# Kernel tuning notes

Measured on AMD Instinct MI355X. Metric: run time of the kernel, lower is better.

Reference implementation:

```python
import jax, jax.numpy as jnp
import numpy as np

SCALE = 16.0 / 8.0  # alpha / rank


def setup_inputs() -> dict:
    key = jax.random.key(0)
    ks = jax.random.split(key, 5)
    d_in, d_out, rank = 4096, 4096, 8
    x = jax.random.normal(ks[0], (4, 2048, d_in), dtype=jnp.float32)
    base_weight = jax.random.normal(ks[1], (d_out, d_in), dtype=jnp.float32) * 0.02
    lora_A = jax.random.normal(ks[2], (rank, d_in), dtype=jnp.float32) * 0.02
    lora_B = jax.random.normal(ks[3], (d_out, rank), dtype=jnp.float32) * 0.02
    bias = jax.random.normal(ks[4], (d_out,), dtype=jnp.float32) * 0.02
    return {"x": x, "base_weight": base_weight, "lora_A": lora_A,
            "lora_B": lora_B, "bias": bias}


def reference(x, base_weight, lora_A, lora_B, bias):
    # weight = base + scale * (B @ A)   -> [d_out, d_in]
    weight = base_weight + SCALE * (lora_B @ lora_A)
    # F.linear: x @ weight.T + bias
    return jnp.einsum('bsi,oi->bso', x, weight) + bias
```

## Files before the change

### kernel.cpp

```cpp
#include <hip/hip_runtime.h>
#include <hip/hip_bf16.h>
#include <cstdio>


using bf16   = __bf16;
using bf16x8 = __attribute__((ext_vector_type(8))) __bf16;
using f32x4  = __attribute__((ext_vector_type(4))) float;

#define BM 256
#define BN 256
#define BK 64

__global__ __launch_bounds__(256) void prep_x(const float* __restrict__ x,
                                              bf16* __restrict__ Xb, long n8) {
    const long stride = (long)gridDim.x * blockDim.x;
    for (long i = (long)blockIdx.x * blockDim.x + threadIdx.x; i < n8; i += stride) {
        const float4 a = reinterpret_cast<const float4*>(x)[2 * i];
        const float4 b = reinterpret_cast<const float4*>(x)[2 * i + 1];
        bf16x8 o;
        o[0] = (bf16)a.x; o[1] = (bf16)a.y; o[2] = (bf16)a.z; o[3] = (bf16)a.w;
        o[4] = (bf16)b.x; o[5] = (bf16)b.y; o[6] = (bf16)b.z; o[7] = (bf16)b.w;
        reinterpret_cast<bf16x8*>(Xb)[i] = o;
    }
}

__global__ __launch_bounds__(256) void prep_w(const float* __restrict__ base,
                                              const float* __restrict__ A,
                                              const float* __restrict__ Bm,
                                              bf16* __restrict__ Wb,
                                              int K, int rank, float scale) {
    const int o = blockIdx.x;
    float br[8];
    const int rr = rank < 8 ? rank : 8;
    for (int r = 0; r < rr; ++r) br[r] = scale * Bm[(size_t)o * rank + r];

    const float* brow = base + (size_t)o * K;
    bf16*        wrow = Wb + (size_t)o * K;

    for (int c = threadIdx.x * 8; c < K; c += 256 * 8) {
        float4 s0 = *reinterpret_cast<const float4*>(brow + c);
        float4 s1 = *reinterpret_cast<const float4*>(brow + c + 4);
        if (rank == 8) {
#pragma unroll
            for (int r = 0; r < 8; ++r) {
                const float4 a0 = *reinterpret_cast<const float4*>(A + (size_t)r * K + c);
                const float4 a1 = *reinterpret_cast<const float4*>(A + (size_t)r * K + c + 4);
                s0.x += br[r] * a0.x; s0.y += br[r] * a0.y;
                s0.z += br[r] * a0.z; s0.w += br[r] * a0.w;
                s1.x += br[r] * a1.x; s1.y += br[r] * a1.y;
                s1.z += br[r] * a1.z; s1.w += br[r] * a1.w;
            }
        } else {
            for (int r = 0; r < rank; ++r) {
                const float b = scale * Bm[(size_t)o * rank + r];
                const float4 a0 = *reinterpret_cast<const float4*>(A + (size_t)r * K + c);
                const float4 a1 = *reinterpret_cast<const float4*>(A + (size_t)r * K + c + 4);
                s0.x += b * a0.x; s0.y += b * a0.y; s0.z += b * a0.z; s0.w += b * a0.w;
                s1.x += b * a1.x; s1.y += b * a1.y; s1.z += b * a1.z; s1.w += b * a1.w;
            }
        }
        bf16x8 ov;
        ov[0] = (bf16)s0.x; ov[1] = (bf16)s0.y; ov[2] = (bf16)s0.z; ov[3] = (bf16)s0.w;
        ov[4] = (bf16)s1.x; ov[5] = (bf16)s1.y; ov[6] = (bf16)s1.z; ov[7] = (bf16)s1.w;
        *reinterpret_cast<bf16x8*>(wrow + c) = ov;
    }
}

__global__ __launch_bounds__(512, 2) void gemm_8ph(
    const bf16* __restrict__ Xb,
    const bf16* __restrict__ Wb,
    const float* __restrict__ bias,
    float* __restrict__ out,
    int M, int N, int K)
{
    __shared__ __align__(16) bf16 As[2 * 2 * 256 * 32];
    __shared__ __align__(16) bf16 Bs[2 * 2 * 256 * 32];

    const int tid  = threadIdx.x;
    const int lane = tid & 63;
    const int wv   = tid >> 6;
    const int wm   = wv >> 2;
    const int wn   = wv & 3;

    const int nbx = gridDim.x;
    const int nwg = gridDim.x * gridDim.y;
    const int orig = blockIdx.y * nbx + blockIdx.x;
    const int swz = ((nwg & 7) == 0) ? ((orig & 7) * (nwg >> 3) + (orig >> 3)) : orig;
    const int m0 = (swz / nbx) * BM;
    const int n0 = (swz % nbx) * BN;

    const int r16 = lane & 15;
    const int q   = lane >> 4;
    const int cq  = (q ^ ((r16 >> 1) & 3)) * 8;

    const bf16* srcA[2];
    const bf16* srcB[2];
#pragma unroll
    for (int i = 0; i < 2; ++i) {
        const int slot = i * 512 + tid;
        const int row  = slot >> 2;
        const int c    = (tid & 3) ^ ((row >> 1) & 3);
        srcA[i] = Xb + (size_t)(m0 + row) * K + c * 8;
        srcB[i] = Wb + (size_t)(n0 + row) * K + c * 8;
    }
    const int dst0 = (0 * 512 + wv * 64) * 8;
    const int dst1 = (1 * 512 + wv * 64) * 8;

#define STAGE_A(buf, kh, koff)                                                        \
    do {                                                                              \
        __builtin_amdgcn_global_load_lds(                                             \
            (const __attribute__((address_space(1))) void*)(srcA[0] + (koff) + (kh) * 32), \
            (__attribute__((address_space(3))) void*)(As + (buf) * 16384 + (kh) * 8192 + dst0), \
            16, 0, 0);                                                                \
        __builtin_amdgcn_global_load_lds(                                             \
            (const __attribute__((address_space(1))) void*)(srcA[1] + (koff) + (kh) * 32), \
            (__attribute__((address_space(3))) void*)(As + (buf) * 16384 + (kh) * 8192 + dst1), \
            16, 0, 0);                                                                \
    } while (0)
#define STAGE_B(buf, kh, koff)                                                        \
    do {                                                                              \
        __builtin_amdgcn_global_load_lds(                                             \
            (const __attribute__((address_space(1))) void*)(srcB[0] + (koff) + (kh) * 32), \
            (__attribute__((address_space(3))) void*)(Bs + (buf) * 16384 + (kh) * 8192 + dst0), \
            16, 0, 0);                                                                \
        __builtin_amdgcn_global_load_lds(                                             \
            (const __attribute__((address_space(1))) void*)(srcB[1] + (koff) + (kh) * 32), \
            (__attribute__((address_space(3))) void*)(Bs + (buf) * 16384 + (kh) * 8192 + dst1), \
            16, 0, 0);                                                                \
    } while (0)

    int aoff[2][4], boff[4];
#pragma unroll
    for (int mh = 0; mh < 2; ++mh)
#pragma unroll
        for (int f = 0; f < 4; ++f)
            aoff[mh][f] = (wm * 128 + mh * 64 + f * 16 + r16) * 32 + cq;
#pragma unroll
    for (int f = 0; f < 4; ++f)
        boff[f] = (wn * 64 + f * 16 + r16) * 32 + cq;

    f32x4 acc[8][4] = {};

    const int NT = K / BK;

    STAGE_A(0, 0, 0);
    STAGE_B(0, 0, 0);
    STAGE_A(0, 1, 0);
    STAGE_B(0, 1, 0);
    if (NT > 1) {
        STAGE_A(1, 0, BK);
        STAGE_B(1, 0, BK);
        asm volatile("s_waitcnt vmcnt(8)" ::: "memory");
    } else {
        asm volatile("s_waitcnt vmcnt(4)" ::: "memory");
    }
    __builtin_amdgcn_s_barrier();

    for (int t = 0; t < NT; ++t) {
        const int cur   = t & 1;
        const int nxt   = cur ^ 1;
        const int koff1 = (t + 1) * BK;
        const int koff2 = (t + 2) * BK;
        const bool pre1 = (t + 1 < NT);
        const bool pre2 = (t + 2 < NT);
        bf16x8 bf[4], af[4];

        {
            const bf16* Ab = As + cur * 16384;
            const bf16* Bb = Bs + cur * 16384;
#pragma unroll
            for (int f = 0; f < 4; ++f) bf[f] = *reinterpret_cast<const bf16x8*>(Bb + boff[f]);
#pragma unroll
            for (int f = 0; f < 4; ++f) af[f] = *reinterpret_cast<const bf16x8*>(Ab + aoff[0][f]);
            if (pre1) STAGE_A(nxt, 1, koff1);
            __builtin_amdgcn_s_barrier();
            asm volatile("s_waitcnt lgkmcnt(0)" ::: "memory");
            __builtin_amdgcn_sched_barrier(0);
            __builtin_amdgcn_s_setprio(1);
#pragma unroll
            for (int f = 0; f < 4; ++f)
#pragma unroll
                for (int n = 0; n < 4; ++n)
                    acc[f][n] = __builtin_amdgcn_mfma_f32_16x16x32_bf16(af[f], bf[n], acc[f][n], 0, 0, 0);
            __builtin_amdgcn_s_setprio(0);
            __builtin_amdgcn_s_barrier();
        }
        {
            const bf16* Ab = As + cur * 16384;
#pragma unroll
            for (int f = 0; f < 4; ++f) af[f] = *reinterpret_cast<const bf16x8*>(Ab + aoff[1][f]);
            if (pre1) STAGE_B(nxt, 1, koff1);
            __builtin_amdgcn_s_barrier();
            asm volatile("s_waitcnt lgkmcnt(0)" ::: "memory");
            __builtin_amdgcn_sched_barrier(0);
            __builtin_amdgcn_s_setprio(1);
#pragma unroll
            for (int f = 0; f < 4; ++f)
#pragma unroll
                for (int n = 0; n < 4; ++n)
                    acc[4 + f][n] = __builtin_amdgcn_mfma_f32_16x16x32_bf16(af[f], bf[n], acc[4 + f][n], 0, 0, 0);
            __builtin_amdgcn_s_setprio(0);
            if (t == NT - 1) asm volatile("s_waitcnt vmcnt(0)" ::: "memory");
            else             asm volatile("s_waitcnt vmcnt(8)" ::: "memory");
            __builtin_amdgcn_s_barrier();
        }
        {
            const bf16* Ab = As + cur * 16384 + 8192;
            const bf16* Bb = Bs + cur * 16384 + 8192;
#pragma unroll
            for (int f = 0; f < 4; ++f) bf[f] = *reinterpret_cast<const bf16x8*>(Bb + boff[f]);
#pragma unroll
            for (int f = 0; f < 4; ++f) af[f] = *reinterpret_cast<const bf16x8*>(Ab + aoff[0][f]);
            if (pre2) STAGE_A(cur, 0, koff2);
            __builtin_amdgcn_s_barrier();
            asm volatile("s_waitcnt lgkmcnt(0)" ::: "memory");
            __builtin_amdgcn_sched_barrier(0);
            __builtin_amdgcn_s_setprio(1);
#pragma unroll
            for (int f = 0; f < 4; ++f)
#pragma unroll
                for (int n = 0; n < 4; ++n)
                    acc[f][n] = __builtin_amdgcn_mfma_f32_16x16x32_bf16(af[f], bf[n], acc[f][n], 0, 0, 0);
            __builtin_amdgcn_s_setprio(0);
            __builtin_amdgcn_s_barrier();
        }
        {
            const bf16* Ab = As + cur * 16384 + 8192;
#pragma unroll
            for (int f = 0; f < 4; ++f) af[f] = *reinterpret_cast<const bf16x8*>(Ab + aoff[1][f]);
            if (pre2) STAGE_B(cur, 0, koff2);
            __builtin_amdgcn_s_barrier();
            asm volatile("s_waitcnt lgkmcnt(0)" ::: "memory");
            __builtin_amdgcn_sched_barrier(0);
            __builtin_amdgcn_s_setprio(1);
#pragma unroll
            for (int f = 0; f < 4; ++f)
#pragma unroll
                for (int n = 0; n < 4; ++n)
                    acc[4 + f][n] = __builtin_amdgcn_mfma_f32_16x16x32_bf16(af[f], bf[n], acc[4 + f][n], 0, 0, 0);
            __builtin_amdgcn_s_setprio(0);
            if (t == NT - 2)     asm volatile("s_waitcnt vmcnt(4)" ::: "memory");
            else if (t < NT - 2) asm volatile("s_waitcnt vmcnt(8)" ::: "memory");
            __builtin_amdgcn_s_barrier();
        }
    }

#pragma unroll
    for (int mf = 0; mf < 8; ++mf) {
        const int gr = m0 + wm * 128 + (mf >> 2) * 64 + (mf & 3) * 16 + q * 4;
#pragma unroll
        for (int nf = 0; nf < 4; ++nf) {
            const int gc = n0 + wn * 64 + nf * 16 + r16;
            const float bv = bias[gc];
#pragma unroll
            for (int r = 0; r < 4; ++r)
                out[(size_t)(gr + r) * N + gc] = acc[mf][nf][r] + bv;
        }
    }
#undef STAGE_A
#undef STAGE_B
}

extern "C" void kernel_launch(void* const* d_in, const int* in_sizes, int n_in,
                              void* d_out, int out_size, void* d_ws, size_t ws_size,
                              hipStream_t stream) {
    const float* x    = (const float*)d_in[0];
    const float* base = (const float*)d_in[1];
    const float* lA   = (const float*)d_in[2];
    const float* lB   = (const float*)d_in[3];
    const float* bias = (const float*)d_in[4];
    float* out = (float*)d_out;

    const int  N    = in_sizes[4];
    const int  rank = in_sizes[3] / N;
    const int  K    = in_sizes[2] / rank;
    const long M    = (long)in_sizes[0] / K;
    const float scale = 16.0f / (float)rank;

    bf16* Xb = (bf16*)d_ws;
    bf16* Wb = Xb + (size_t)M * K;
    const size_t need = ((size_t)M * K + (size_t)N * K) * sizeof(bf16);
    if (ws_size < need) {
        fprintf(stderr, "kernel_launch: ws_size %zu < needed %zu\n", ws_size, need);
        return;
    }

    const long n8x = (long)M * K / 8;
    long blk = (n8x + 255) / 256;
    if (blk > 2048) blk = 2048;
    prep_x<<<dim3((unsigned)blk), dim3(256), 0, stream>>>(x, Xb, n8x);

    prep_w<<<dim3((unsigned)N), dim3(256), 0, stream>>>(base, lA, lB, Wb, K, rank, scale);

    gemm_8ph<<<dim3(N / BN, (unsigned)(M / BM)), dim3(512), 0, stream>>>(
        Xb, Wb, bias, out, (int)M, N, K);
}
```

Before: 541.9 us.

## Merge GEMM phases to two per k-step and fuse the prep kernels

The GEMM main loop now runs two phases per k-step instead of four. Both A fragment sets are loaded into separate registers (af0/af1), and the A and B prefetches for a stage are issued together. A partial lgkmcnt wait lets the first MFMA group start before the second A fragment arrives. This halves the block barriers per iteration and overlaps LDS reads with MFMA issue, at the cost of more live VGPRs under the 512x2 launch bound, which risks spills. The x conversion and weight merge kernels are also fused into one launch split by block index, removing one launch gap.

```diff
diff --git a/kernel.cpp b/kernel.cpp
--- a/kernel.cpp
+++ b/kernel.cpp
@@ -10,63 +10,63 @@
 #define BM 256
 #define BN 256
 #define BK 64
-
-__global__ __launch_bounds__(256) void prep_x(const float* __restrict__ x,
-                                              bf16* __restrict__ Xb, long n8) {
-    const long stride = (long)gridDim.x * blockDim.x;
-    for (long i = (long)blockIdx.x * blockDim.x + threadIdx.x; i < n8; i += stride) {
-        const float4 a = reinterpret_cast<const float4*>(x)[2 * i];
-        const float4 b = reinterpret_cast<const float4*>(x)[2 * i + 1];
-        bf16x8 o;
-        o[0] = (bf16)a.x; o[1] = (bf16)a.y; o[2] = (bf16)a.z; o[3] = (bf16)a.w;
-        o[4] = (bf16)b.x; o[5] = (bf16)b.y; o[6] = (bf16)b.z; o[7] = (bf16)b.w;
-        reinterpret_cast<bf16x8*>(Xb)[i] = o;
+#define WXBLK 2048
+
+__global__ __launch_bounds__(256) void prep_fused(
+    const float* __restrict__ x, const float* __restrict__ base,
+    const float* __restrict__ A, const float* __restrict__ Bm,
+    bf16* __restrict__ Xb, bf16* __restrict__ Wb,
+    long n8x, int K, int rank, float scale) {
+    if (blockIdx.x < WXBLK) {
+        const long stride = (long)WXBLK * 256;
+        for (long i = (long)blockIdx.x * 256 + threadIdx.x; i < n8x; i += stride) {
+            const float4 a = reinterpret_cast<const float4*>(x)[2 * i];
+            const float4 b = reinterpret_cast<const float4*>(x)[2 * i + 1];
+            bf16x8 o;
+            o[0] = (bf16)a.x; o[1] = (bf16)a.y; o[2] = (bf16)a.z; o[3] = (bf16)a.w;
+            o[4] = (bf16)b.x; o[5] = (bf16)b.y; o[6] = (bf16)b.z; o[7] = (bf16)b.w;
+            reinterpret_cast<bf16x8*>(Xb)[i] = o;
+        }
+    } else {
+        const int o = blockIdx.x - WXBLK;
+        float br[8];
+        const int rr = rank < 8 ? rank : 8;
+        for (int r = 0; r < rr; ++r) br[r] = scale * Bm[(size_t)o * rank + r];
+
+        const float* brow = base + (size_t)o * K;
+        bf16*        wrow = Wb + (size_t)o * K;
+
+        for (int c = threadIdx.x * 8; c < K; c += 256 * 8) {
+            float4 s0 = *reinterpret_cast<const float4*>(brow + c);
+            float4 s1 = *reinterpret_cast<const float4*>(brow + c + 4);
+            if (rank == 8) {
+#pragma unroll
+                for (int r = 0; r < 8; ++r) {
+                    const float4 a0 = *reinterpret_cast<const float4*>(A + (size_t)r * K + c);
+                    const float4 a1 = *reinterpret_cast<const float4*>(A + (size_t)r * K + c + 4);
+                    s0.x += br[r] * a0.x; s0.y += br[r] * a0.y;
+                    s0.z += br[r] * a0.z; s0.w += br[r] * a0.w;
+                    s1.x += br[r] * a1.x; s1.y += br[r] * a1.y;
+                    s1.z += br[r] * a1.z; s1.w += br[r] * a1.w;
+                }
+            } else {
+                for (int r = 0; r < rank; ++r) {
+                    const float b = scale * Bm[(size_t)o * rank + r];
+                    const float4 a0 = *reinterpret_cast<const float4*>(A + (size_t)r * K + c);
+                    const float4 a1 = *reinterpret_cast<const float4*>(A + (size_t)r * K + c + 4);
+                    s0.x += b * a0.x; s0.y += b * a0.y; s0.z += b * a0.z; s0.w += b * a0.w;
+                    s1.x += b * a1.x; s1.y += b * a1.y; s1.z += b * a1.z; s1.w += b * a1.w;
+                }
+            }
+            bf16x8 ov;
+            ov[0] = (bf16)s0.x; ov[1] = (bf16)s0.y; ov[2] = (bf16)s0.z; ov[3] = (bf16)s0.w;
+            ov[4] = (bf16)s1.x; ov[5] = (bf16)s1.y; ov[6] = (bf16)s1.z; ov[7] = (bf16)s1.w;
+            *reinterpret_cast<bf16x8*>(wrow + c) = ov;
+        }
     }
 }
 
-__global__ __launch_bounds__(256) void prep_w(const float* __restrict__ base,
-                                              const float* __restrict__ A,
-                                              const float* __restrict__ Bm,
-                                              bf16* __restrict__ Wb,
-                                              int K, int rank, float scale) {
-    const int o = blockIdx.x;
-    float br[8];
-    const int rr = rank < 8 ? rank : 8;
-    for (int r = 0; r < rr; ++r) br[r] = scale * Bm[(size_t)o * rank + r];
-
-    const float* brow = base + (size_t)o * K;
-    bf16*        wrow = Wb + (size_t)o * K;
-
-    for (int c = threadIdx.x * 8; c < K; c += 256 * 8) {
-        float4 s0 = *reinterpret_cast<const float4*>(brow + c);
-        float4 s1 = *reinterpret_cast<const float4*>(brow + c + 4);
-        if (rank == 8) {
-#pragma unroll
-            for (int r = 0; r < 8; ++r) {
-                const float4 a0 = *reinterpret_cast<const float4*>(A + (size_t)r * K + c);
-                const float4 a1 = *reinterpret_cast<const float4*>(A + (size_t)r * K + c + 4);
-                s0.x += br[r] * a0.x; s0.y += br[r] * a0.y;
-                s0.z += br[r] * a0.z; s0.w += br[r] * a0.w;
-                s1.x += br[r] * a1.x; s1.y += br[r] * a1.y;
-                s1.z += br[r] * a1.z; s1.w += br[r] * a1.w;
-            }
-        } else {
-            for (int r = 0; r < rank; ++r) {
-                const float b = scale * Bm[(size_t)o * rank + r];
-                const float4 a0 = *reinterpret_cast<const float4*>(A + (size_t)r * K + c);
-                const float4 a1 = *reinterpret_cast<const float4*>(A + (size_t)r * K + c + 4);
-                s0.x += b * a0.x; s0.y += b * a0.y; s0.z += b * a0.z; s0.w += b * a0.w;
-                s1.x += b * a1.x; s1.y += b * a1.y; s1.z += b * a1.z; s1.w += b * a1.w;
-            }
-        }
-        bf16x8 ov;
-        ov[0] = (bf16)s0.x; ov[1] = (bf16)s0.y; ov[2] = (bf16)s0.z; ov[3] = (bf16)s0.w;
-        ov[4] = (bf16)s1.x; ov[5] = (bf16)s1.y; ov[6] = (bf16)s1.z; ov[7] = (bf16)s1.w;
-        *reinterpret_cast<bf16x8*>(wrow + c) = ov;
-    }
-}
-
-__global__ __launch_bounds__(512, 2) void gemm_8ph(
+__global__ __launch_bounds__(512, 2) void gemm_2reg(
     const bf16* __restrict__ Xb,
     const bf16* __restrict__ Wb,
     const float* __restrict__ bias,
@@ -163,17 +163,27 @@
         const int koff2 = (t + 2) * BK;
         const bool pre1 = (t + 1 < NT);
         const bool pre2 = (t + 2 < NT);
-        bf16x8 bf[4], af[4];
+        bf16x8 bf[4], af0[4], af1[4];
 
         {
             const bf16* Ab = As + cur * 16384;
             const bf16* Bb = Bs + cur * 16384;
 #pragma unroll
-            for (int f = 0; f < 4; ++f) bf[f] = *reinterpret_cast<const bf16x8*>(Bb + boff[f]);
-#pragma unroll
-            for (int f = 0; f < 4; ++f) af[f] = *reinterpret_cast<const bf16x8*>(Ab + aoff[0][f]);
-            if (pre1) STAGE_A(nxt, 1, koff1);
-            __builtin_amdgcn_s_barrier();
+            for (int f = 0; f < 4; ++f) bf[f]  = *reinterpret_cast<const bf16x8*>(Bb + boff[f]);
+#pragma unroll
+            for (int f = 0; f < 4; ++f) af0[f] = *reinterpret_cast<const bf16x8*>(Ab + aoff[0][f]);
+#pragma unroll
+            for (int f = 0; f < 4; ++f) af1[f] = *reinterpret_cast<const bf16x8*>(Ab + aoff[1][f]);
+            if (pre1) { STAGE_A(nxt, 1, koff1); STAGE_B(nxt, 1, koff1); }
+            asm volatile("s_waitcnt lgkmcnt(4)" ::: "memory");
+            __builtin_amdgcn_sched_barrier(0);
+            __builtin_amdgcn_s_setprio(1);
+#pragma unroll
+            for (int f = 0; f < 4; ++f)
+#pragma unroll
+                for (int n = 0; n < 4; ++n)
+                    acc[f][n] = __builtin_amdgcn_mfma_f32_16x16x32_bf16(af0[f], bf[n], acc[f][n], 0, 0, 0);
+            __builtin_amdgcn_s_setprio(0);
             asm volatile("s_waitcnt lgkmcnt(0)" ::: "memory");
             __builtin_amdgcn_sched_barrier(0);
             __builtin_amdgcn_s_setprio(1);
@@ -181,24 +191,7 @@
             for (int f = 0; f < 4; ++f)
 #pragma unroll
                 for (int n = 0; n < 4; ++n)
-                    acc[f][n] = __builtin_amdgcn_mfma_f32_16x16x32_bf16(af[f], bf[n], acc[f][n], 0, 0, 0);
-            __builtin_amdgcn_s_setprio(0);
-            __builtin_amdgcn_s_barrier();
-        }
-        {
-            const bf16* Ab = As + cur * 16384;
-#pragma unroll
-            for (int f = 0; f < 4; ++f) af[f] = *reinterpret_cast<const bf16x8*>(Ab + aoff[1][f]);
-            if (pre1) STAGE_B(nxt, 1, koff1);
-            __builtin_amdgcn_s_barrier();
-            asm volatile("s_waitcnt lgkmcnt(0)" ::: "memory");
-            __builtin_amdgcn_sched_barrier(0);
-            __builtin_amdgcn_s_setprio(1);
-#pragma unroll
-            for (int f = 0; f < 4; ++f)
-#pragma unroll
-                for (int n = 0; n < 4; ++n)
-                    acc[4 + f][n] = __builtin_amdgcn_mfma_f32_16x16x32_bf16(af[f], bf[n], acc[4 + f][n], 0, 0, 0);
+                    acc[4 + f][n] = __builtin_amdgcn_mfma_f32_16x16x32_bf16(af1[f], bf[n], acc[4 + f][n], 0, 0, 0);
             __builtin_amdgcn_s_setprio(0);
             if (t == NT - 1) asm volatile("s_waitcnt vmcnt(0)" ::: "memory");
             else             asm volatile("s_waitcnt vmcnt(8)" ::: "memory");
@@ -208,11 +201,21 @@
             const bf16* Ab = As + cur * 16384 + 8192;
             const bf16* Bb = Bs + cur * 16384 + 8192;
 #pragma unroll
-            for (int f = 0; f < 4; ++f) bf[f] = *reinterpret_cast<const bf16x8*>(Bb + boff[f]);
-#pragma unroll
-            for (int f = 0; f < 4; ++f) af[f] = *reinterpret_cast<const bf16x8*>(Ab + aoff[0][f]);
-            if (pre2) STAGE_A(cur, 0, koff2);
-            __builtin_amdgcn_s_barrier();
+            for (int f = 0; f < 4; ++f) bf[f]  = *reinterpret_cast<const bf16x8*>(Bb + boff[f]);
+#pragma unroll
+            for (int f = 0; f < 4; ++f) af0[f] = *reinterpret_cast<const bf16x8*>(Ab + aoff[0][f]);
+#pragma unroll
+            for (int f = 0; f < 4; ++f) af1[f] = *reinterpret_cast<const bf16x8*>(Ab + aoff[1][f]);
+            if (pre2) { STAGE_A(cur, 0, koff2); STAGE_B(cur, 0, koff2); }
+            asm volatile("s_waitcnt lgkmcnt(4)" ::: "memory");
+            __builtin_amdgcn_sched_barrier(0);
+            __builtin_amdgcn_s_setprio(1);
+#pragma unroll
+            for (int f = 0; f < 4; ++f)
+#pragma unroll
+                for (int n = 0; n < 4; ++n)
+                    acc[f][n] = __builtin_amdgcn_mfma_f32_16x16x32_bf16(af0[f], bf[n], acc[f][n], 0, 0, 0);
+            __builtin_amdgcn_s_setprio(0);
             asm volatile("s_waitcnt lgkmcnt(0)" ::: "memory");
             __builtin_amdgcn_sched_barrier(0);
             __builtin_amdgcn_s_setprio(1);
@@ -220,28 +223,11 @@
             for (int f = 0; f < 4; ++f)
 #pragma unroll
                 for (int n = 0; n < 4; ++n)
-                    acc[f][n] = __builtin_amdgcn_mfma_f32_16x16x32_bf16(af[f], bf[n], acc[f][n], 0, 0, 0);
-            __builtin_amdgcn_s_setprio(0);
-            __builtin_amdgcn_s_barrier();
-        }
-        {
-            const bf16* Ab = As + cur * 16384 + 8192;
-#pragma unroll
-            for (int f = 0; f < 4; ++f) af[f] = *reinterpret_cast<const bf16x8*>(Ab + aoff[1][f]);
-            if (pre2) STAGE_B(cur, 0, koff2);
-            __builtin_amdgcn_s_barrier();
-            asm volatile("s_waitcnt lgkmcnt(0)" ::: "memory");
-            __builtin_amdgcn_sched_barrier(0);
-            __builtin_amdgcn_s_setprio(1);
-#pragma unroll
-            for (int f = 0; f < 4; ++f)
-#pragma unroll
-                for (int n = 0; n < 4; ++n)
-                    acc[4 + f][n] = __builtin_amdgcn_mfma_f32_16x16x32_bf16(af[f], bf[n], acc[4 + f][n], 0, 0, 0);
+                    acc[4 + f][n] = __builtin_amdgcn_mfma_f32_16x16x32_bf16(af1[f], bf[n], acc[4 + f][n], 0, 0, 0);
             __builtin_amdgcn_s_setprio(0);
             if (t == NT - 2)     asm volatile("s_waitcnt vmcnt(4)" ::: "memory");
             else if (t < NT - 2) asm volatile("s_waitcnt vmcnt(8)" ::: "memory");
-            __builtin_amdgcn_s_barrier();
+            if (t < NT - 1) __builtin_amdgcn_s_barrier();
         }
     }
 
@@ -286,12 +272,9 @@
     }
 
     const long n8x = (long)M * K / 8;
-    long blk = (n8x + 255) / 256;
-    if (blk > 2048) blk = 2048;
-    prep_x<<<dim3((unsigned)blk), dim3(256), 0, stream>>>(x, Xb, n8x);
-
-    prep_w<<<dim3((unsigned)N), dim3(256), 0, stream>>>(base, lA, lB, Wb, K, rank, scale);
-
-    gemm_8ph<<<dim3(N / BN, (unsigned)(M / BM)), dim3(512), 0, stream>>>(
+    prep_fused<<<dim3((unsigned)(WXBLK + N)), dim3(256), 0, stream>>>(
+        x, base, lA, lB, Xb, Wb, n8x, K, rank, scale);
+
+    gemm_2reg<<<dim3(N / BN, (unsigned)(M / BM)), dim3(512), 0, stream>>>(
         Xb, Wb, bias, out, (int)M, N, K);
 }
```

Measured after the change: 553.3 us. +2.1%, slower.
